# Kernel tuning notes

Measured on AMD Instinct MI355X. Metric: run time of the kernel, lower is better.

Reference implementation:

```python
import jax, jax.numpy as jnp
import numpy as np
from jax import lax

NUM_PATHS = 16384
NUM_EDGES = 4096
LINK_DIM = 128   # link_state_dim (GRU input dim)
PATH_DIM = 128   # path_state_dim (GRU units)
MAX_LEN = 20     # max path length (static scatter shape)


def setup_inputs() -> dict:
    key = jax.random.key(0)
    ks = jax.random.split(key, 8)
    rng = np.random.default_rng(0)
    lens_np = rng.integers(4, MAX_LEN + 1, size=NUM_PATHS)
    lens_np[0] = MAX_LEN  # ensure max_len is reached
    total = int(lens_np.sum())
    idx_np = np.repeat(np.arange(NUM_PATHS), lens_np)
    offsets = np.repeat(np.concatenate([[0], np.cumsum(lens_np)[:-1]]), lens_np)
    seqs_np = np.arange(total) - offsets
    paths_np = rng.integers(0, NUM_EDGES, size=total)
    scale = 0.05
    return {
        "inputs": jax.random.normal(ks[0], (NUM_EDGES, LINK_DIM), jnp.float32),
        "paths": jnp.asarray(paths_np, jnp.int32),
        "idx": jnp.asarray(idx_np, jnp.int32),
        "seqs": jnp.asarray(seqs_np, jnp.int32),
        "lens": jnp.asarray(lens_np, jnp.int32),
        "gru_kernel": jax.random.normal(ks[1], (LINK_DIM, 3 * PATH_DIM), jnp.float32) * scale,
        "gru_rkernel": jax.random.normal(ks[2], (PATH_DIM, 3 * PATH_DIM), jnp.float32) * scale,
        "gru_bias": jax.random.normal(ks[3], (2, 3 * PATH_DIM), jnp.float32) * scale,
        "wq": jax.random.normal(ks[4], (PATH_DIM, PATH_DIM), jnp.float32) * scale,
        "wk": jax.random.normal(ks[5], (PATH_DIM, PATH_DIM), jnp.float32) * scale,
        "wv": jax.random.normal(ks[6], (PATH_DIM, PATH_DIM), jnp.float32) * scale,
    }


def _pem_forward(inputs, paths, idx, seqs, lens, gru_kernel, gru_rkernel, gru_bias, wq, wk, wv):
    P = lens.shape[0]
    D = gru_rkernel.shape[0]
    # gather per-step edge states and pack into padded [P, L, Din] sequences
    h_tild = inputs[paths]                                        # [T, Din]
    link_inputs = jnp.zeros((P, MAX_LEN, inputs.shape[1]), inputs.dtype)
    link_inputs = link_inputs.at[idx, seqs].set(h_tild)

    mask = jnp.arange(MAX_LEN, dtype=lens.dtype)[:, None] < lens[None, :]  # [L, P]
    xs = jnp.swapaxes(link_inputs, 0, 1)                          # [L, P, Din]

    def step(h, inp):
        x, m = inp
        xz, xr, xh = jnp.split(x @ gru_kernel + gru_bias[0], 3, axis=-1)
        hz, hr, hh = jnp.split(h @ gru_rkernel + gru_bias[1], 3, axis=-1)
        z = jax.nn.sigmoid(xz + hz)
        r = jax.nn.sigmoid(xr + hr)
        cand = jnp.tanh(xh + r * hh)
        h_new = z * h + (1.0 - z) * cand
        m2 = m[:, None]
        h_next = jnp.where(m2, h_new, h)        # carry state past sequence end
        y = jnp.where(m2, h_new, 0.0)           # zero outputs past sequence end
        return h_next, y

    h0 = jnp.zeros((P, D), inputs.dtype)
    last_state, hs = lax.scan(step, h0, (xs, mask))
    hidden_states = jnp.swapaxes(hs, 0, 1)                        # [P, L, D]

    key_ = jnp.einsum('pld,de->ple', hidden_states, wk)
    query = last_state @ wq                                       # [P, D]
    value = jnp.einsum('pld,de->ple', hidden_states, wv)
    att = jnp.einsum('pld,pd->pl', key_, query)                   # no softmax (as in source)
    context = jnp.einsum('pl,pld->pd', att, value)[:, None, :]    # [P, 1, D]
    return context


def reference(inputs, paths, idx, seqs, lens, gru_kernel, gru_rkernel, gru_bias, wq, wk, wv):
    return _pem_forward(inputs, paths, idx, seqs, lens,
                        gru_kernel, gru_rkernel, gru_bias, wq, wk, wv)
```

## Files before the change

kernel.cpp:

```cpp
#include <hip/hip_runtime.h>
#include <cstdint>

#define NP 16384
#define NE 4096
#define DIM 128
#define ML 20
#define TP 16
#define NT (NP/TP)

typedef _Float16 f16;
typedef _Float16 f16x8 __attribute__((ext_vector_type(8)));
typedef _Float16 f16x2 __attribute__((ext_vector_type(2)));
typedef float    f32x4 __attribute__((ext_vector_type(4)));

__global__ __launch_bounds__(1024) void k_sort(const int* __restrict__ lens,
                                               int* __restrict__ perm) {
    __shared__ int cnt[ML + 1];
    const int tid = threadIdx.x;
    if (tid <= ML) cnt[tid] = 0;
    __syncthreads();
    for (int p = tid; p < NP; p += 1024) atomicAdd(&cnt[lens[p]], 1);
    __syncthreads();
    if (tid == 0) {
        int s = 0;
        for (int i = ML; i >= 0; --i) { int c = cnt[i]; cnt[i] = s; s += c; }
    }
    __syncthreads();
    for (int p = tid; p < NP; p += 1024) {
        int pos = atomicAdd(&cnt[lens[p]], 1);
        perm[pos] = p;
    }
}

__global__ void k_prep(const int* __restrict__ idx, const int* __restrict__ seqs,
                       const int* __restrict__ paths, int total,
                       const float* __restrict__ inputs,
                       const float* __restrict__ gk, const float* __restrict__ gr,
                       int* __restrict__ edge_map, f16* __restrict__ inx,
                       f16* __restrict__ btz, f16* __restrict__ btr,
                       f16* __restrict__ btcx, f16* __restrict__ btch) {
    const int i = blockIdx.x * 256 + threadIdx.x;
    if (i < total) edge_map[idx[i] * ML + seqs[i]] = paths[i];
    inx[i] = (f16)inputs[i];
    if (i < 16384) {
        const int n = i >> 7, k = i & 127;
        btz[n*256 + k]       = (f16)gk[k*384 + n];
        btz[n*256 + 128 + k] = (f16)gr[k*384 + n];
        btr[n*256 + k]       = (f16)gk[k*384 + 128 + n];
        btr[n*256 + 128 + k] = (f16)gr[k*384 + 128 + n];
        btcx[n*128 + k]      = (f16)gk[k*384 + 256 + n];
        btch[n*128 + k]      = (f16)gr[k*384 + 256 + n];
    }
}

__device__ __forceinline__ float frcp(float x)  { return __builtin_amdgcn_rcpf(x); }
__device__ __forceinline__ float fsig(float x)  { return frcp(1.f + __expf(-x)); }
__device__ __forceinline__ float ftanh(float x) { float e = __expf(2.f * x); return 1.f - 2.f * frcp(e + 1.f); }


__global__ __launch_bounds__(512, 2) void k_gru(
    const f16* __restrict__ inx, const int* __restrict__ lens,
    const f16* __restrict__ btz, const f16* __restrict__ btr,
    const f16* __restrict__ btcx, const f16* __restrict__ btch,
    const float* __restrict__ gb, const int* __restrict__ edge_map,
    const int* __restrict__ perm, f16* __restrict__ hs, float* __restrict__ last)
{
    __shared__ f16 H16[2][TP * DIM];
    __shared__ int pgs[TP], lns[TP];

    const int tid  = threadIdx.x;
    const int lane = tid & 63;
    const int w    = tid >> 6;
    const int nw   = w * 16;
    const int arow = lane & 15;
    const int agrp = lane >> 4;
    const int d    = nw + arow;

    if (tid < TP) { int pg = perm[blockIdx.x * TP + tid]; pgs[tid] = pg; lns[tid] = lens[pg]; }
    for (int i = tid; i < TP * DIM; i += 512) H16[0][i] = (f16)0.f;
    asm volatile("s_waitcnt lgkmcnt(0)" ::: "memory");
    __builtin_amdgcn_s_barrier();

    int tmax = 0;
    #pragma unroll
    for (int i = 0; i < TP; ++i) tmax = max(tmax, lns[i]);

    f16x8 Bz[8], Br[8], Bx[4], Bh[4];
    {
        const int cb = d * 256 + agrp * 8;
        #pragma unroll
        for (int ks = 0; ks < 8; ++ks) {
            Bz[ks] = *(const f16x8*)(btz + cb + ks * 32);
            Br[ks] = *(const f16x8*)(btr + cb + ks * 32);
        }
        const int cc = d * 128 + agrp * 8;
        #pragma unroll
        for (int ks = 0; ks < 4; ++ks) {
            Bx[ks] = *(const f16x8*)(btcx + cc + ks * 32);
            Bh[ks] = *(const f16x8*)(btch + cc + ks * 32);
        }
    }

    const float bzc = gb[d]       + gb[384 + d];
    const float brc = gb[128 + d] + gb[512 + d];
    const float bxc = gb[256 + d];
    const float bhc = gb[640 + d];

    float hold[4] = {0.f, 0.f, 0.f, 0.f};
    int ln4[4], hsrow[4], h16a[4], pg4[4];
    #pragma unroll
    for (int r = 0; r < 4; ++r) {
        const int p = agrp * 4 + r;
        ln4[r]   = lns[p];
        pg4[r]   = pgs[p];
        hsrow[r] = pgs[p] * ML;
        h16a[r]  = p * DIM + (((d >> 3) ^ (p & 7)) * 8) + (d & 7);
    }

    const int ep = pgs[arow] * ML;

    f16x8 xa[4];
    int e_nxt;
    {
        const int e0 = edge_map[ep] & (NE - 1);
        const f16* xp = inx + e0 * DIM + agrp * 8;
        #pragma unroll
        for (int ks = 0; ks < 4; ++ks) xa[ks] = *(const f16x8*)(xp + ks * 32);
        e_nxt = edge_map[ep + ((1 < ML) ? 1 : 0)];
    }

    for (int t = 0; t < tmax; ++t) {
        const f16* Hc = &H16[t & 1][0];
        f16*       Hn = &H16[(t & 1) ^ 1][0];

        f16x8 ha[4];
        #pragma unroll
        for (int ks = 0; ks < 4; ++ks) {
            const int chunk = (ks * 4 + agrp) ^ (arow & 7);
            ha[ks] = *(const f16x8*)(Hc + arow * DIM + chunk * 8);
        }

        f32x4 Az = {0.f,0.f,0.f,0.f}, Ar = {0.f,0.f,0.f,0.f};
        f32x4 Ax = {0.f,0.f,0.f,0.f}, Ah = {0.f,0.f,0.f,0.f};
        #pragma unroll
        for (int ks = 0; ks < 4; ++ks) {
            Az = __builtin_amdgcn_mfma_f32_16x16x32_f16(xa[ks], Bz[ks], Az, 0, 0, 0);
            Ar = __builtin_amdgcn_mfma_f32_16x16x32_f16(xa[ks], Br[ks], Ar, 0, 0, 0);
            Ax = __builtin_amdgcn_mfma_f32_16x16x32_f16(xa[ks], Bx[ks], Ax, 0, 0, 0);
        }
        #pragma unroll
        for (int ks = 0; ks < 4; ++ks) {
            Az = __builtin_amdgcn_mfma_f32_16x16x32_f16(ha[ks], Bz[4 + ks], Az, 0, 0, 0);
            Ar = __builtin_amdgcn_mfma_f32_16x16x32_f16(ha[ks], Br[4 + ks], Ar, 0, 0, 0);
            Ah = __builtin_amdgcn_mfma_f32_16x16x32_f16(ha[ks], Bh[ks],     Ah, 0, 0, 0);
        }

        {
            const int e = e_nxt & (NE - 1);
            const f16* xp = inx + e * DIM + agrp * 8;
            #pragma unroll
            for (int ks = 0; ks < 4; ++ks) xa[ks] = *(const f16x8*)(xp + ks * 32);
            const int tn2 = (t + 2 < ML) ? (t + 2) : (ML - 1);
            e_nxt = edge_map[ep + tn2];
        }

        #pragma unroll
        for (int r = 0; r < 4; ++r) {
            const float z  = fsig(Az[r] + bzc);
            const float rg = fsig(Ar[r] + brc);
            const float c  = ftanh(Ax[r] + bxc + rg * (Ah[r] + bhc));
            const float hn = z * hold[r] + (1.f - z) * c;
            hold[r] = (t < ln4[r]) ? hn : hold[r];
            const f16 hv = (f16)hold[r];
            Hn[h16a[r]] = hv;
            hs[(hsrow[r] + t) * DIM + d] = hv;
        }

        asm volatile("s_waitcnt lgkmcnt(0)" ::: "memory");
        __builtin_amdgcn_s_barrier();
    }

    #pragma unroll
    for (int r = 0; r < 4; ++r)
        last[pg4[r] * DIM + d] = hold[r];
}


__global__ __launch_bounds__(256, 2) void k_qkq(
    const float* __restrict__ last, const float* __restrict__ wq,
    const float* __restrict__ wk, float* __restrict__ kq)
{
    __shared__ float LT[DIM][64];
    __shared__ float QT[DIM][64];
    const int tid = threadIdx.x;
    const int pb = blockIdx.x * 64;
    {
        const int p  = tid >> 2;
        const int dd = (tid & 3) * 32;
        const float4* src = (const float4*)(last + (pb + p) * DIM + dd);
        #pragma unroll
        for (int q = 0; q < 8; ++q) {
            float4 v = src[q];
            LT[dd + q * 4 + 0][p] = v.x; LT[dd + q * 4 + 1][p] = v.y;
            LT[dd + q * 4 + 2][p] = v.z; LT[dd + q * 4 + 3][p] = v.w;
        }
    }
    __syncthreads();
    const int e0 = (tid & 63) * 2;
    const int p0 = (tid >> 6) * 16;
    float a0[16], a1[16];
    #pragma unroll
    for (int i = 0; i < 16; ++i) { a0[i] = a1[i] = 0.f; }
    for (int dd = 0; dd < DIM; ++dd) {
        const float2 ww = *(const float2*)(wq + dd * DIM + e0);
        #pragma unroll
        for (int i = 0; i < 16; ++i) {
            const float lv = LT[dd][p0 + i];
            a0[i] = fmaf(lv, ww.x, a0[i]);
            a1[i] = fmaf(lv, ww.y, a1[i]);
        }
    }
    #pragma unroll
    for (int i = 0; i < 16; ++i) { QT[e0][p0 + i] = a0[i]; QT[e0 + 1][p0 + i] = a1[i]; }
    __syncthreads();
    float b0a[16], b1a[16];
    #pragma unroll
    for (int i = 0; i < 16; ++i) { b0a[i] = b1a[i] = 0.f; }
    for (int e = 0; e < DIM; ++e) {
        const float w0 = wk[e0 * DIM + e];
        const float w1 = wk[(e0 + 1) * DIM + e];
        #pragma unroll
        for (int i = 0; i < 16; ++i) {
            const float qv = QT[e][p0 + i];
            b0a[i] = fmaf(qv, w0, b0a[i]);
            b1a[i] = fmaf(qv, w1, b1a[i]);
        }
    }
    #pragma unroll
    for (int i = 0; i < 16; ++i) {
        float2 o; o.x = b0a[i]; o.y = b1a[i];
        *(float2*)(kq + (pb + p0 + i) * DIM + e0) = o;
    }
}


__global__ __launch_bounds__(256) void k_attn(
    const f16* __restrict__ hs, const float* __restrict__ kq,
    const int* __restrict__ lens, const float* __restrict__ wv,
    float* __restrict__ out)
{
    __shared__ float ctx[4][DIM];
    const int tid  = threadIdx.x;
    const int wave = tid >> 6;
    const int lane = tid & 63;
    const int p    = blockIdx.x * 4 + wave;
    const int ln   = lens[p];
    const float2 kqv = *(const float2*)(kq + p * DIM + lane * 2);
    float c0 = 0.f, c1 = 0.f;
    for (int l = 0; l < ln; ++l) {
        const f16x2 h2 = *(const f16x2*)(hs + (p * ML + l) * DIM + lane * 2);
        const float hx = (float)h2.x, hy = (float)h2.y;
        float s = hx * kqv.x + hy * kqv.y;
        #pragma unroll
        for (int off = 32; off > 0; off >>= 1) s += __shfl_xor(s, off, 64);
        c0 = fmaf(s, hx, c0);
        c1 = fmaf(s, hy, c1);
    }
    ctx[wave][lane * 2]     = c0;
    ctx[wave][lane * 2 + 1] = c1;
    __syncthreads();
    const int ee = lane * 2;
    float o0 = 0.f, o1 = 0.f;
    for (int dd = 0; dd < DIM; ++dd) {
        const float cv = ctx[wave][dd];
        const float2 ww = *(const float2*)(wv + dd * DIM + ee);
        o0 = fmaf(cv, ww.x, o0);
        o1 = fmaf(cv, ww.y, o1);
    }
    float2 o; o.x = o0; o.y = o1;
    *(float2*)(out + p * DIM + ee) = o;
}


extern "C" void kernel_launch(void* const* d_in, const int* in_sizes, int n_in,
                              void* d_out, int out_size, void* d_ws, size_t ws_size,
                              hipStream_t stream)
{
    const float* inputs = (const float*)d_in[0];
    const int*   paths  = (const int*)d_in[1];
    const int*   idx    = (const int*)d_in[2];
    const int*   seqs   = (const int*)d_in[3];
    const int*   lens   = (const int*)d_in[4];
    const float* gk     = (const float*)d_in[5];
    const float* gr     = (const float*)d_in[6];
    const float* gb     = (const float*)d_in[7];
    const float* wq     = (const float*)d_in[8];
    const float* wk     = (const float*)d_in[9];
    const float* wv     = (const float*)d_in[10];
    float* out = (float*)d_out;
    const int total = in_sizes[1];

    float* last = (float*)d_ws;
    float* kq   = last + (size_t)NP * DIM;
    f16*   hs   = (f16*)(kq + (size_t)NP * DIM);
    f16*   inx  = hs + (size_t)NP * ML * DIM;
    f16*   btz  = inx + (size_t)NE * DIM;
    f16*   btr  = btz + 128 * 256;
    f16*   btcx = btr + 128 * 256;
    f16*   btch = btcx + 128 * 128;
    int* edge_map = (int*)(btch + 128 * 128);
    int* perm   = edge_map + NP * ML;

    k_sort<<<1, 1024, 0, stream>>>(lens, perm);
    k_prep<<<(NE * DIM) / 256, 256, 0, stream>>>(idx, seqs, paths, total, inputs,
                                                 gk, gr, edge_map, inx,
                                                 btz, btr, btcx, btch);
    k_gru<<<NT, 512, 0, stream>>>(inx, lens, btz, btr, btcx, btch, gb, edge_map, perm, hs, last);
    k_qkq<<<NP / 64, 256, 0, stream>>>(last, wq, wk, kq);
    k_attn<<<NP / 4, 256, 0, stream>>>(hs, kq, lens, wv, out);
}
```

Measured before the change: 290.1 us.

## Process two 16-path tiles per GRU block and use per-wave sort counters

The GRU recurrence kernel now handles 32 paths per block as two interleaved 16-row MFMA tiles. This reuses the register-resident weight fragments across twice the work and gives independent MFMA chains to hide latency within each sequential time step. The counting sort now uses per-wavefront histograms with a prefix pass, which reduces shared-memory atomic contention. In exchange, the GRU kernel uses more registers, which may lower occupancy, and the grid has half as many blocks.

```diff
diff --git a/kernel.cpp b/kernel.cpp
--- a/kernel.cpp
+++ b/kernel.cpp
@@ -5,7 +5,7 @@
 #define NE 4096
 #define DIM 128
 #define ML 20
-#define TP 16
+#define TP 32
 #define NT (NP/TP)
 
 typedef _Float16 f16;
@@ -15,19 +15,42 @@
 
 __global__ __launch_bounds__(1024) void k_sort(const int* __restrict__ lens,
                                                int* __restrict__ perm) {
-    __shared__ int cnt[ML + 1];
+    __shared__ int wcnt[16][33];
+    __shared__ int start[ML + 1];
     const int tid = threadIdx.x;
-    if (tid <= ML) cnt[tid] = 0;
-    __syncthreads();
-    for (int p = tid; p < NP; p += 1024) atomicAdd(&cnt[lens[p]], 1);
+    const int wv  = tid >> 6;
+    for (int i = tid; i < 16 * 33; i += 1024) ((int*)wcnt)[i] = 0;
+    __syncthreads();
+    #pragma unroll
+    for (int k = 0; k < NP / 1024; ++k) {
+        const int p = k * 1024 + tid;
+        atomicAdd(&wcnt[wv][lens[p]], 1);
+    }
     __syncthreads();
     if (tid == 0) {
         int s = 0;
-        for (int i = ML; i >= 0; --i) { int c = cnt[i]; cnt[i] = s; s += c; }
-    }
-    __syncthreads();
-    for (int p = tid; p < NP; p += 1024) {
-        int pos = atomicAdd(&cnt[lens[p]], 1);
+        for (int i = ML; i >= 0; --i) {
+            int c = 0;
+            #pragma unroll
+            for (int w2 = 0; w2 < 16; ++w2) c += wcnt[w2][i];
+            start[i] = s; s += c;
+        }
+    }
+    __syncthreads();
+    if (tid <= ML) {
+        int running = start[tid];
+        #pragma unroll
+        for (int w2 = 0; w2 < 16; ++w2) {
+            int tmp = wcnt[w2][tid];
+            wcnt[w2][tid] = running;
+            running += tmp;
+        }
+    }
+    __syncthreads();
+    #pragma unroll
+    for (int k = 0; k < NP / 1024; ++k) {
+        const int p = k * 1024 + tid;
+        int pos = atomicAdd(&wcnt[wv][lens[p]], 1);
         perm[pos] = p;
     }
 }
@@ -106,74 +129,109 @@
     const float bxc = gb[256 + d];
     const float bhc = gb[640 + d];
 
-    float hold[4] = {0.f, 0.f, 0.f, 0.f};
-    int ln4[4], hsrow[4], h16a[4], pg4[4];
+    float hold0[4] = {0.f,0.f,0.f,0.f}, hold1[4] = {0.f,0.f,0.f,0.f};
+    int ln0[4], ln1[4], hsr0[4], hsr1[4], h16a0[4], h16a1[4], pg0[4], pg1[4];
     #pragma unroll
     for (int r = 0; r < 4; ++r) {
-        const int p = agrp * 4 + r;
-        ln4[r]   = lns[p];
-        pg4[r]   = pgs[p];
-        hsrow[r] = pgs[p] * ML;
-        h16a[r]  = p * DIM + (((d >> 3) ^ (p & 7)) * 8) + (d & 7);
-    }
-
-    const int ep = pgs[arow] * ML;
-
-    f16x8 xa[4];
-    int e_nxt;
+        const int pa = agrp * 4 + r;
+        const int pb = 16 + pa;
+        ln0[r] = lns[pa];            ln1[r] = lns[pb];
+        pg0[r] = pgs[pa];            pg1[r] = pgs[pb];
+        hsr0[r] = pgs[pa] * ML;      hsr1[r] = pgs[pb] * ML;
+        h16a0[r] = pa * DIM + (((d >> 3) ^ (pa & 7)) * 8) + (d & 7);
+        h16a1[r] = pb * DIM + (((d >> 3) ^ (pb & 7)) * 8) + (d & 7);
+    }
+
+    const int ep0 = pgs[arow] * ML;
+    const int ep1 = pgs[16 + arow] * ML;
+
+    f16x8 xa0[4], xa1[4];
+    int en0, en1;
     {
-        const int e0 = edge_map[ep] & (NE - 1);
-        const f16* xp = inx + e0 * DIM + agrp * 8;
-        #pragma unroll
-        for (int ks = 0; ks < 4; ++ks) xa[ks] = *(const f16x8*)(xp + ks * 32);
-        e_nxt = edge_map[ep + ((1 < ML) ? 1 : 0)];
+        const int e0 = edge_map[ep0] & (NE - 1);
+        const int e1 = edge_map[ep1] & (NE - 1);
+        const f16* xp0 = inx + e0 * DIM + agrp * 8;
+        const f16* xp1 = inx + e1 * DIM + agrp * 8;
+        #pragma unroll
+        for (int ks = 0; ks < 4; ++ks) {
+            xa0[ks] = *(const f16x8*)(xp0 + ks * 32);
+            xa1[ks] = *(const f16x8*)(xp1 + ks * 32);
+        }
+        en0 = edge_map[ep0 + 1];
+        en1 = edge_map[ep1 + 1];
     }
 
     for (int t = 0; t < tmax; ++t) {
         const f16* Hc = &H16[t & 1][0];
         f16*       Hn = &H16[(t & 1) ^ 1][0];
 
-        f16x8 ha[4];
+        f16x8 ha0[4], ha1[4];
         #pragma unroll
         for (int ks = 0; ks < 4; ++ks) {
             const int chunk = (ks * 4 + agrp) ^ (arow & 7);
-            ha[ks] = *(const f16x8*)(Hc + arow * DIM + chunk * 8);
-        }
-
-        f32x4 Az = {0.f,0.f,0.f,0.f}, Ar = {0.f,0.f,0.f,0.f};
-        f32x4 Ax = {0.f,0.f,0.f,0.f}, Ah = {0.f,0.f,0.f,0.f};
-        #pragma unroll
-        for (int ks = 0; ks < 4; ++ks) {
-            Az = __builtin_amdgcn_mfma_f32_16x16x32_f16(xa[ks], Bz[ks], Az, 0, 0, 0);
-            Ar = __builtin_amdgcn_mfma_f32_16x16x32_f16(xa[ks], Br[ks], Ar, 0, 0, 0);
-            Ax = __builtin_amdgcn_mfma_f32_16x16x32_f16(xa[ks], Bx[ks], Ax, 0, 0, 0);
-        }
-        #pragma unroll
-        for (int ks = 0; ks < 4; ++ks) {
-            Az = __builtin_amdgcn_mfma_f32_16x16x32_f16(ha[ks], Bz[4 + ks], Az, 0, 0, 0);
-            Ar = __builtin_amdgcn_mfma_f32_16x16x32_f16(ha[ks], Br[4 + ks], Ar, 0, 0, 0);
-            Ah = __builtin_amdgcn_mfma_f32_16x16x32_f16(ha[ks], Bh[ks],     Ah, 0, 0, 0);
+            ha0[ks] = *(const f16x8*)(Hc + arow * DIM + chunk * 8);
+            ha1[ks] = *(const f16x8*)(Hc + (16 + arow) * DIM + chunk * 8);
+        }
+
+        f32x4 Az0 = {0.f,0.f,0.f,0.f}, Ar0 = {0.f,0.f,0.f,0.f};
+        f32x4 Ax0 = {0.f,0.f,0.f,0.f}, Ah0 = {0.f,0.f,0.f,0.f};
+        f32x4 Az1 = {0.f,0.f,0.f,0.f}, Ar1 = {0.f,0.f,0.f,0.f};
+        f32x4 Ax1 = {0.f,0.f,0.f,0.f}, Ah1 = {0.f,0.f,0.f,0.f};
+        #pragma unroll
+        for (int ks = 0; ks < 4; ++ks) {
+            Az0 = __builtin_amdgcn_mfma_f32_16x16x32_f16(xa0[ks], Bz[ks], Az0, 0, 0, 0);
+            Az1 = __builtin_amdgcn_mfma_f32_16x16x32_f16(xa1[ks], Bz[ks], Az1, 0, 0, 0);
+            Ar0 = __builtin_amdgcn_mfma_f32_16x16x32_f16(xa0[ks], Br[ks], Ar0, 0, 0, 0);
+            Ar1 = __builtin_amdgcn_mfma_f32_16x16x32_f16(xa1[ks], Br[ks], Ar1, 0, 0, 0);
+            Ax0 = __builtin_amdgcn_mfma_f32_16x16x32_f16(xa0[ks], Bx[ks], Ax0, 0, 0, 0);
+            Ax1 = __builtin_amdgcn_mfma_f32_16x16x32_f16(xa1[ks], Bx[ks], Ax1, 0, 0, 0);
+        }
+        #pragma unroll
+        for (int ks = 0; ks < 4; ++ks) {
+            Az0 = __builtin_amdgcn_mfma_f32_16x16x32_f16(ha0[ks], Bz[4 + ks], Az0, 0, 0, 0);
+            Az1 = __builtin_amdgcn_mfma_f32_16x16x32_f16(ha1[ks], Bz[4 + ks], Az1, 0, 0, 0);
+            Ar0 = __builtin_amdgcn_mfma_f32_16x16x32_f16(ha0[ks], Br[4 + ks], Ar0, 0, 0, 0);
+            Ar1 = __builtin_amdgcn_mfma_f32_16x16x32_f16(ha1[ks], Br[4 + ks], Ar1, 0, 0, 0);
+            Ah0 = __builtin_amdgcn_mfma_f32_16x16x32_f16(ha0[ks], Bh[ks],     Ah0, 0, 0, 0);
+            Ah1 = __builtin_amdgcn_mfma_f32_16x16x32_f16(ha1[ks], Bh[ks],     Ah1, 0, 0, 0);
         }
 
         {
-            const int e = e_nxt & (NE - 1);
-            const f16* xp = inx + e * DIM + agrp * 8;
+            const int e0 = en0 & (NE - 1);
+            const int e1 = en1 & (NE - 1);
+            const f16* xp0 = inx + e0 * DIM + agrp * 8;
+            const f16* xp1 = inx + e1 * DIM + agrp * 8;
             #pragma unroll
-            for (int ks = 0; ks < 4; ++ks) xa[ks] = *(const f16x8*)(xp + ks * 32);
+            for (int ks = 0; ks < 4; ++ks) {
+                xa0[ks] = *(const f16x8*)(xp0 + ks * 32);
+                xa1[ks] = *(const f16x8*)(xp1 + ks * 32);
+            }
             const int tn2 = (t + 2 < ML) ? (t + 2) : (ML - 1);
-            e_nxt = edge_map[ep + tn2];
+            en0 = edge_map[ep0 + tn2];
+            en1 = edge_map[ep1 + tn2];
         }
 
         #pragma unroll
         for (int r = 0; r < 4; ++r) {
-            const float z  = fsig(Az[r] + bzc);
-            const float rg = fsig(Ar[r] + brc);
-            const float c  = ftanh(Ax[r] + bxc + rg * (Ah[r] + bhc));
-            const float hn = z * hold[r] + (1.f - z) * c;
-            hold[r] = (t < ln4[r]) ? hn : hold[r];
-            const f16 hv = (f16)hold[r];
-            Hn[h16a[r]] = hv;
-            hs[(hsrow[r] + t) * DIM + d] = hv;
+            const float z  = fsig(Az0[r] + bzc);
+            const float rg = fsig(Ar0[r] + brc);
+            const float c  = ftanh(Ax0[r] + bxc + rg * (Ah0[r] + bhc));
+            const float hn = z * hold0[r] + (1.f - z) * c;
+            hold0[r] = (t < ln0[r]) ? hn : hold0[r];
+            const f16 hv = (f16)hold0[r];
+            Hn[h16a0[r]] = hv;
+            hs[(hsr0[r] + t) * DIM + d] = hv;
+        }
+        #pragma unroll
+        for (int r = 0; r < 4; ++r) {
+            const float z  = fsig(Az1[r] + bzc);
+            const float rg = fsig(Ar1[r] + brc);
+            const float c  = ftanh(Ax1[r] + bxc + rg * (Ah1[r] + bhc));
+            const float hn = z * hold1[r] + (1.f - z) * c;
+            hold1[r] = (t < ln1[r]) ? hn : hold1[r];
+            const f16 hv = (f16)hold1[r];
+            Hn[h16a1[r]] = hv;
+            hs[(hsr1[r] + t) * DIM + d] = hv;
         }
 
         asm volatile("s_waitcnt lgkmcnt(0)" ::: "memory");
@@ -181,8 +239,10 @@
     }
 
     #pragma unroll
-    for (int r = 0; r < 4; ++r)
-        last[pg4[r] * DIM + d] = hold[r];
+    for (int r = 0; r < 4; ++r) {
+        last[pg0[r] * DIM + d] = hold0[r];
+        last[pg1[r] * DIM + d] = hold1[r];
+    }
 }
 
 
```

Result: faster. 282.4 us (-2.7%).
